# Optimization experiments

Hardware: AMD Instinct MI355X
Metric: run time of the kernel (lower is better)

The kernel has to match this reference:

```python
import jax, jax.numpy as jnp
import numpy as np

N_LINKS = 100000
N_EDGES = 1600000
D = 64          # link_state_dim
RU = 256        # readout_units
G = 256         # number of graphs
T = 4           # message passing iterations


def _glorot(key, shape):
    fan_in, fan_out = shape[0], shape[1]
    limit = np.sqrt(6.0 / (fan_in + fan_out)).astype(np.float32)
    return jax.random.uniform(key, shape, jnp.float32, -limit, limit)


def setup_inputs() -> dict:
    key = jax.random.key(0)
    ks = jax.random.split(key, 12)
    states_action = jax.random.normal(ks[0], (N_LINKS, D), jnp.float32)
    states_graph_ids = jnp.sort(jax.random.randint(ks[1], (N_LINKS,), 0, G))
    states_first = jax.random.randint(ks[2], (N_EDGES,), 0, N_LINKS)
    states_second = jax.random.randint(ks[3], (N_EDGES,), 0, N_LINKS)
    # Message: Dense(2D -> D) with selu
    W_msg = _glorot(ks[4], (2 * D, D)); b_msg = jnp.zeros((D,), jnp.float32)
    # GCN: Linear(D -> D) + relu, then unsorted_segment_sum
    W_gcn = _glorot(ks[5], (D, D)); b_gcn = jnp.zeros((D,), jnp.float32)
    # Readout MLP: D -> RU -> RU -> 1
    W_r1 = _glorot(ks[6], (D, RU)); b_r1 = jnp.zeros((RU,), jnp.float32)
    W_r2 = _glorot(ks[7], (RU, RU)); b_r2 = jnp.zeros((RU,), jnp.float32)
    W_r3 = _glorot(ks[8], (RU, 1)); b_r3 = jnp.zeros((1,), jnp.float32)
    return {
        "states_action": states_action,
        "W_msg": W_msg, "b_msg": b_msg,
        "W_gcn": W_gcn, "b_gcn": b_gcn,
        "W_r1": W_r1, "b_r1": b_r1,
        "W_r2": W_r2, "b_r2": b_r2,
        "W_r3": W_r3, "b_r3": b_r3,
        "states_graph_ids": states_graph_ids,
        "states_first": states_first,
        "states_second": states_second,
        "sates_num_edges": N_EDGES,
    }


def reference(states_action, W_msg, b_msg, W_gcn, b_gcn,
              W_r1, b_r1, W_r2, b_r2, W_r3, b_r3,
              states_graph_ids, states_first, states_second, sates_num_edges):
    n_links = states_action.shape[0]
    link_state = states_action
    for _ in range(T):
        main_e = link_state[states_first]      # [E, D]
        neigh_e = link_state[states_second]    # [E, D]
        concat = jnp.concatenate([main_e, neigh_e], axis=1)  # [E, 2D]
        msg = jax.nn.selu(concat @ W_msg + b_msg)            # [E, D]
        h = jax.nn.relu(msg @ W_gcn + b_gcn)                 # [E, D]
        # scatter-add messages back onto links (segment ids = states_second)
        link_state = jax.ops.segment_sum(h, states_second, num_segments=n_links)
        # dropout rate is 0.0 -> identity
    # per-graph readout (graph ids are sorted, fixed G segments)
    graph_emb = jax.ops.segment_sum(link_state, states_graph_ids, num_segments=G)
    r = jax.nn.selu(graph_emb @ W_r1 + b_r1)
    r = jax.nn.selu(r @ W_r2 + b_r2)
    r = r @ W_r3 + b_r3                                      # [G, 1]
    return r
```

## Files before the change

### kernel.cpp

```cpp
#include <hip/hip_runtime.h>
#include <hip/hip_bf16.h>
#include <math.h>

#define D 64
#define RU 256
#define CHUNK 8
#define QSTRIDE 68
#define BIN_SHIFT 7
#define NSB 256

#if __has_builtin(__builtin_amdgcn_exp2f)
#define EXP2F(x) __builtin_amdgcn_exp2f(x)
#else
#define EXP2F(x) exp2f(x)
#endif

typedef short bf16x8 __attribute__((ext_vector_type(8)));
typedef float f32x4 __attribute__((ext_vector_type(4)));

__device__ __forceinline__ float selu_f(float x) {
    return x > 0.0f ? 1.0507009873554805f * x
                    : 1.7580993408473766f * (__expf(x) - 1.0f);
}

__device__ __forceinline__ float selu_x2(float x2) {
    const float p = fmaxf(x2, 0.0f);
    const float n = fminf(x2, 0.0f);
    const float e = EXP2F(n);
    return fmaf(1.7580993408473766f, e, fmaf(0.72829042516f, p, -1.7580993408473766f));
}

__device__ __forceinline__ short f2bf_rtne(float x) {
    union { float f; unsigned u; } v; v.f = x;
    unsigned r = (v.u + 0x7FFFu + ((v.u >> 16) & 1u)) >> 16;
    return (short)r;
}
__device__ __forceinline__ float bf2f(short s) {
    union { float f; unsigned u; } v; v.u = ((unsigned)(unsigned short)s) << 16;
    return v.f;
}
__device__ __forceinline__ unsigned packpair(float a, float b) {
    float2 p; p.x = a; p.y = b;
    __hip_bfloat162 hb = __float22bfloat162_rn(p);
    return *(unsigned*)&hb;
}

__device__ __forceinline__ bf16x8 pack8(const float* v) {
    union { bf16x8 v; unsigned u[4]; } H;
#pragma unroll
    for (int j = 0; j < 4; ++j) H.u[j] = packpair(v[2 * j], v[2 * j + 1]);
    return H.v;
}

#define FIDX(ks, jt, qd, m) ((((((ks) * 4 + (jt)) * 4 + (qd)) * 16) + (m)) * 8)

__global__ __launch_bounds__(256) void wprep_kernel(
    const float* __restrict__ W_msg, const float* __restrict__ W_gcn,
    const float* __restrict__ b_gcn,
    unsigned short* __restrict__ WAh, unsigned short* __restrict__ WAl,
    unsigned short* __restrict__ WBh, unsigned short* __restrict__ WBl,
    unsigned short* __restrict__ WGh, float* __restrict__ cstar,
    unsigned short* __restrict__ Pb, int n_links)
{
    const float LOG2E = 1.4426950408889634f;
    const int t = blockIdx.x * 256 + threadIdx.x;

    if (blockIdx.x == 0 && threadIdx.x < 64) {
        const int col = threadIdx.x;
        Pb[(size_t)n_links * 64 + col] = 0xFF80;
        const float c0 = bf2f(f2bf_rtne(-1.7580993408473766f));
        float acc = b_gcn[col];
        for (int k = 0; k < 64; ++k)
            acc = fmaf(c0, bf2f(f2bf_rtne(W_gcn[k * 64 + col])), acc);
        cstar[col] = fmaxf(acc, 0.0f);
    }

    if (t >= 4096) return;
    const int i  = t & 7;
    const int m  = (t >> 3) & 15;
    const int qd = (t >> 7) & 3;
    const int jt = (t >> 9) & 3;
    const int ks = t >> 11;
    const int kk = ks * 32 + qd * 8 + i;
    const int nn = jt * 16 + m;

    float w = W_msg[kk * 64 + nn] * LOG2E;
    short hi = f2bf_rtne(w);
    WAh[t] = (unsigned short)hi;
    WAl[t] = (unsigned short)f2bf_rtne(w - bf2f(hi));

    w = W_msg[(64 + kk) * 64 + nn] * LOG2E;
    hi = f2bf_rtne(w);
    WBh[t] = (unsigned short)hi;
    WBl[t] = (unsigned short)f2bf_rtne(w - bf2f(hi));

    WGh[t] = (unsigned short)f2bf_rtne(W_gcn[kk * 64 + nn]);
}

__global__ __launch_bounds__(256) void s2bf_kernel(
    const float* __restrict__ in, unsigned short* __restrict__ out, int n4)
{
    for (int i = blockIdx.x * 256 + threadIdx.x; i < n4; i += gridDim.x * 256) {
        const float4 v = ((const float4*)in)[i];
        uint2 o;
        o.x = packpair(v.x, v.y);
        o.y = packpair(v.z, v.w);
        ((uint2*)out)[i] = o;
    }
}


__global__ __launch_bounds__(256) void histA_kernel(
    const int* __restrict__ second, int* __restrict__ ghist,
    int n_edges, int nbins)
{
    __shared__ int lhist[1024];
    for (int i = threadIdx.x; i < nbins; i += 256) lhist[i] = 0;
    __syncthreads();
    const int per = (n_edges + gridDim.x - 1) / gridDim.x;
    const int e0 = blockIdx.x * per;
    const int e1 = min(e0 + per, n_edges);
    for (int e = e0 + threadIdx.x; e < e1; e += 256)
        atomicAdd(&lhist[second[e] >> BIN_SHIFT], 1);
    __syncthreads();
    for (int i = threadIdx.x; i < nbins; i += 256)
        ghist[i * gridDim.x + blockIdx.x] = lhist[i];
}

__global__ __launch_bounds__(64) void sumbins_kernel(
    int* __restrict__ ghist, int* __restrict__ btot, int nbins)
{
    const int b = blockIdx.x, tid = threadIdx.x;
    int d[4], p[4];
#pragma unroll
    for (int k = 0; k < 4; ++k) {
        d[k] = ghist[b * NSB + k * 64 + tid];
        p[k] = d[k];
    }
#pragma unroll
    for (int off = 1; off < 64; off <<= 1) {
#pragma unroll
        for (int k = 0; k < 4; ++k) {
            const int t = __shfl_up(p[k], off, 64);
            if (tid >= off) p[k] += t;
        }
    }
    int base = 0;
#pragma unroll
    for (int k = 0; k < 4; ++k) {
        const int tot = __shfl(p[k], 63, 64);
        ghist[b * NSB + k * 64 + tid] = base + p[k] - d[k];
        base += tot;
    }
    if (tid == 63) btot[b] = base;
}

__global__ __launch_bounds__(1024) void scanS_kernel(int* __restrict__ data, int n)
{
    __shared__ int wsum[16], woff[16];
    const int tid = threadIdx.x, wave = tid >> 6, lane = tid & 63;
    const int x = (tid < n) ? data[tid] : 0;
    int v = x;
#pragma unroll
    for (int off = 1; off < 64; off <<= 1) {
        const int t = __shfl_up(v, off, 64);
        if (lane >= off) v += t;
    }
    if (lane == 63) wsum[wave] = v;
    __syncthreads();
    if (wave == 0) {
        int s = (lane < 16) ? wsum[lane] : 0;
#pragma unroll
        for (int off = 1; off < 16; off <<= 1) {
            const int t = __shfl_up(s, off, 64);
            if (lane >= off) s += t;
        }
        if (lane < 16) woff[lane] = s - wsum[lane];
    }
    __syncthreads();
    if (tid < n) data[tid] = woff[wave] + v - x;
}

__global__ __launch_bounds__(256) void scatterC_kernel(
    const int* __restrict__ first, const int* __restrict__ second,
    const int* __restrict__ ghist, const int* __restrict__ btot,
    unsigned* __restrict__ tmp, int n_edges, int nbins)
{
    __shared__ int lcur[1024];
    for (int i = threadIdx.x; i < nbins; i += 256)
        lcur[i] = ghist[i * NSB + blockIdx.x] + btot[i];
    __syncthreads();
    const int per = (n_edges + gridDim.x - 1) / gridDim.x;
    const int e0 = blockIdx.x * per;
    const int e1 = min(e0 + per, n_edges);
    for (int e = e0 + threadIdx.x; e < e1; e += 256) {
        const int s = second[e];
        const int pos = atomicAdd(&lcur[s >> BIN_SHIFT], 1);
        tmp[pos] = (unsigned)first[e] | ((unsigned)(s & 127) << 20);
    }
}

__global__ __launch_bounds__(256) void binsortD_kernel(
    const unsigned* __restrict__ tmp, const int* __restrict__ btot,
    int* __restrict__ sfirst, int* __restrict__ row_ptr, int* __restrict__ ptot,
    int n_edges, int n_links, int nbins)
{
    __shared__ int ldeg[128];
    __shared__ int lpre[128];
    __shared__ int lcur[128];
    const int b = blockIdx.x;
    const int tid = threadIdx.x;
    const int lbase = b << BIN_SHIFT;
    const int nl = min(128, n_links - lbase);
    const int eb = btot[b];
    const int ee = (b + 1 < nbins) ? btot[b + 1] : n_edges;

    if (tid < 128) ldeg[tid] = 0;
    __syncthreads();
    for (int e = eb + tid; e < ee; e += 256)
        atomicAdd(&ldeg[tmp[e] >> 20], 1);
    __syncthreads();
    if (tid < 64) {
        const int d0 = ldeg[tid], d1 = ldeg[64 + tid];
        int p0 = d0, p1 = d1;
#pragma unroll
        for (int off = 1; off < 64; off <<= 1) {
            const int t0 = __shfl_up(p0, off, 64);
            const int t1 = __shfl_up(p1, off, 64);
            if (tid >= off) { p0 += t0; p1 += t1; }
        }
        const int tot0 = __shfl(p0, 63, 64);
        lpre[tid] = p0 - d0;
        lpre[64 + tid] = tot0 + p1 - d1;
        const int n0 = (d0 + 15) >> 4, n1 = (d1 + 15) >> 4;
        int q0 = n0, q1 = n1;
#pragma unroll
        for (int off = 1; off < 64; off <<= 1) {
            const int t0 = __shfl_up(q0, off, 64);
            const int t1 = __shfl_up(q1, off, 64);
            if (tid >= off) { q0 += t0; q1 += t1; }
        }
        if (tid == 63) ptot[b] = q0 + q1;
    }
    __syncthreads();
    if (tid < nl) row_ptr[lbase + tid] = eb + lpre[tid];
    if (b == nbins - 1 && tid == 0) row_ptr[n_links] = n_edges;
    if (tid < 128) lcur[tid] = lpre[tid];
    __syncthreads();
    for (int e = eb + tid; e < ee; e += 256) {
        const unsigned v = tmp[e];
        const int pos = eb + atomicAdd(&lcur[v >> 20], 1);
        sfirst[pos] = (int)(v & 0xFFFFFu);
    }
    if (b == 0)
        for (int i = tid; i < 64; i += 256) sfirst[n_edges + i] = 0;
}

__global__ __launch_bounds__(256) void tbuild_kernel(
    const int* __restrict__ row_ptr, const int* __restrict__ tbase,
    int* __restrict__ ptile, int* __restrict__ tinfo,
    int n_links, int nbins)
{
    __shared__ int rpl[130];
    __shared__ int ltp[130];
    const int b = blockIdx.x, tid = threadIdx.x;
    const int lbase = b << BIN_SHIFT;
    const int nl = min(128, n_links - lbase);
    if (tid <= nl) rpl[tid] = row_ptr[lbase + tid];
    __syncthreads();
    if (tid < 64) {
        const int d0 = (tid < nl) ? rpl[tid + 1] - rpl[tid] : 0;
        const int d1 = (64 + tid < nl) ? rpl[64 + tid + 1] - rpl[64 + tid] : 0;
        const int n0 = (d0 + 15) >> 4, n1 = (d1 + 15) >> 4;
        int p0 = n0, p1 = n1;
#pragma unroll
        for (int off = 1; off < 64; off <<= 1) {
            const int t0 = __shfl_up(p0, off, 64);
            const int t1 = __shfl_up(p1, off, 64);
            if (tid >= off) { p0 += t0; p1 += t1; }
        }
        const int tot0 = __shfl(p0, 63, 64);
        ltp[tid] = p0 - n0;
        ltp[64 + tid] = tot0 + p1 - n1;
        if (tid == 63) ltp[128] = tot0 + p1;
    }
    __syncthreads();
    const int tb = tbase[b];
    if (tid <= nl) ptile[lbase + tid] = tb + ltp[tid];
    const int ntb = ltp[128];
    for (int tl = tid; tl < ntb; tl += 256) {
        int lo = 0, hi = nl - 1;
        while (lo < hi) {
            const int mid = (lo + hi + 1) >> 1;
            if (ltp[mid] <= tl) lo = mid; else hi = mid - 1;
        }
        const int li = lo;
        const int eo = rpl[li] + ((tl - ltp[li]) << 4);
        const int rend = rpl[li + 1];
        const int vc = min(16, rend - eo);
        const int last = (eo + 16 >= rend) ? 1 : 0;
        tinfo[tb + tl] = eo | ((li & 7) << 21) | (last << 24) | (vc << 25);
    }
    if (b == nbins - 1 && tid < 8) tinfo[tb + ntb + tid] = 0;
}

__global__ __launch_bounds__(256) void growfind_kernel(
    const int* __restrict__ gid, int* __restrict__ grow, int n_links, int G)
{
    const int g = blockIdx.x * blockDim.x + threadIdx.x;
    if (g > G) return;
    if (g == G) { grow[G] = n_links; return; }
    int lo = 0, hi = n_links;
    while (lo < hi) {
        const int mid = (lo + hi) >> 1;
        if (gid[mid] < g) lo = mid + 1; else hi = mid;
    }
    grow[g] = lo;
}

__global__ __launch_bounds__(256) void p_mfma_kernel(
    const unsigned short* __restrict__ Sb,
    const unsigned short* __restrict__ WAh, const unsigned short* __restrict__ WAl,
    unsigned short* __restrict__ P, int n_links)
{
    const int tid = threadIdx.x;
    const int wave = tid >> 6;
    const int lane = tid & 63;
    const int m = lane & 15;
    const int qd = lane >> 4;

    bf16x8 Bh[2][4], Bl[2][4];
#pragma unroll
    for (int ks = 0; ks < 2; ++ks)
#pragma unroll
        for (int jt = 0; jt < 4; ++jt) {
            const int off = FIDX(ks, jt, qd, m);
            Bh[ks][jt] = *(const bf16x8*)(WAh + off);
            Bl[ks][jt] = *(const bf16x8*)(WAl + off);
        }
    const bf16x8 z = (bf16x8){0, 0, 0, 0, 0, 0, 0, 0};

    const int ngroups = (n_links + 63) >> 6;
    for (int g = blockIdx.x; g < ngroups; g += gridDim.x) {
        const int base = g * 64 + wave * 16;
        const int l = base + m;
        bf16x8 Ah0 = z, Ah1 = z;
        if (l < n_links) {
            Ah0 = *(const bf16x8*)(Sb + (size_t)l * D + qd * 8);
            Ah1 = *(const bf16x8*)(Sb + (size_t)l * D + 32 + qd * 8);
        }
        f32x4 accP[4];
#pragma unroll
        for (int jt = 0; jt < 4; ++jt) {
            accP[jt] = (f32x4){0.f, 0.f, 0.f, 0.f};
            accP[jt] = __builtin_amdgcn_mfma_f32_16x16x32_bf16(Ah0, Bh[0][jt], accP[jt], 0, 0, 0);
            accP[jt] = __builtin_amdgcn_mfma_f32_16x16x32_bf16(Ah0, Bl[0][jt], accP[jt], 0, 0, 0);
            accP[jt] = __builtin_amdgcn_mfma_f32_16x16x32_bf16(Ah1, Bh[1][jt], accP[jt], 0, 0, 0);
            accP[jt] = __builtin_amdgcn_mfma_f32_16x16x32_bf16(Ah1, Bl[1][jt], accP[jt], 0, 0, 0);
        }
#pragma unroll
        for (int r = 0; r < 4; ++r) {
            const int lr = base + qd * 4 + r;
            if (lr < n_links) {
#pragma unroll
                for (int jt = 0; jt < 4; ++jt)
                    P[(size_t)lr * D + jt * 16 + m] =
                        (unsigned short)f2bf_rtne(accP[jt][r]);
            }
        }
    }
}

__global__ __launch_bounds__(256, 4) void edge_link_kernel(
    unsigned short* __restrict__ Sb, const unsigned short* __restrict__ P,
    const int* __restrict__ sfirst, const int* __restrict__ tinfo,
    const int* __restrict__ ptile,
    const float* __restrict__ b_msg,
    const unsigned short* __restrict__ WBh, const unsigned short* __restrict__ WBl,
    const unsigned short* __restrict__ WGh,
    const float* __restrict__ b_gcn, const float* __restrict__ cstar,
    int n_links)
{
    __shared__ float qt[4][CHUNK * QSTRIDE + 4];
    __shared__ float cbl[64];
    const int tid = threadIdx.x;
    const int wave = tid >> 6;
    const int lane = tid & 63;
    const int m = lane & 15;
    const int qd = lane >> 4;

    cbl[lane] = cstar[lane];

    const int l0 = (blockIdx.x * 4 + wave) * CHUNK;
    if (l0 >= n_links) return;
    const int nl = min(CHUNK, n_links - l0);

    const float LOG2E = 1.4426950408889634f;
    float bmsgC[4];
#pragma unroll
    for (int jt = 0; jt < 4; ++jt) bmsgC[jt] = b_msg[jt * 16 + m] * LOG2E;

    {
        const bf16x8 z = (bf16x8){0, 0, 0, 0, 0, 0, 0, 0};
        const int l = l0 + m;
        bf16x8 Ah0 = z, Ah1 = z;
        if ((l < n_links) && (m < CHUNK)) {
            Ah0 = *(const bf16x8*)(Sb + (size_t)l * D + qd * 8);
            Ah1 = *(const bf16x8*)(Sb + (size_t)l * D + 32 + qd * 8);
        }
        f32x4 accQ[4];
#pragma unroll
        for (int jt = 0; jt < 4; ++jt) accQ[jt] = (f32x4){0.f, 0.f, 0.f, 0.f};
#pragma unroll
        for (int ks = 0; ks < 2; ++ks) {
            bf16x8 WbH[4], WbL[4];
#pragma unroll
            for (int jt = 0; jt < 4; ++jt) {
                const int off = FIDX(ks, jt, qd, m);
                WbH[jt] = *(const bf16x8*)(WBh + off);
                WbL[jt] = *(const bf16x8*)(WBl + off);
            }
            const bf16x8 A = ks ? Ah1 : Ah0;
#pragma unroll
            for (int jt = 0; jt < 4; ++jt) {
                accQ[jt] = __builtin_amdgcn_mfma_f32_16x16x32_bf16(A, WbH[jt], accQ[jt], 0, 0, 0);
                accQ[jt] = __builtin_amdgcn_mfma_f32_16x16x32_bf16(A, WbL[jt], accQ[jt], 0, 0, 0);
            }
        }
#pragma unroll
        for (int r = 0; r < 4; ++r) {
            const int row = qd * 4 + r;
            if (row < CHUNK) {
#pragma unroll
                for (int jt = 0; jt < 4; ++jt)
                    qt[wave][row * QSTRIDE + jt * 16 + m] = accQ[jt][r] + bmsgC[jt];
            }
        }
    }

    bf16x8 Gh[2][4];
#pragma unroll
    for (int ks = 0; ks < 2; ++ks)
#pragma unroll
        for (int jt = 0; jt < 4; ++jt)
            Gh[ks][jt] = *(const bf16x8*)(WGh + FIDX(ks, jt, qd, m));

    float bias_gcn[4];
#pragma unroll
    for (int jt = 0; jt < 4; ++jt) bias_gcn[jt] = b_gcn[jt * 16 + m];

    const int tpv = ptile[l0 + min(lane, nl)];
#pragma unroll
    for (int i = 0; i < CHUNK; ++i) {
        if (i < nl && __shfl(tpv, i + 1, 64) == __shfl(tpv, i, 64))
            Sb[(size_t)(l0 + i) * D + lane] = 0;
    }
    const int tbeg = __builtin_amdgcn_readfirstlane(tpv);
    const int tend = __builtin_amdgcn_readfirstlane(__shfl(tpv, nl, 64));
    if (tbeg >= tend) return;

    int ti0 = tinfo[tbeg];
    int ti1 = tinfo[tbeg + 1];
    int ti2 = tinfo[tbeg + 2];

    bf16x8 p00, p01;
    {
        const int eo = ti0 & 0x1FFFFF, vc = (ti0 >> 25) & 31;
        int sf = sfirst[eo + m];
        sf = (m < vc) ? sf : n_links;
        const unsigned short* Pr = P + (size_t)sf * D;
        p00 = *(const bf16x8*)(Pr + qd * 8);
        p01 = *(const bf16x8*)(Pr + 32 + qd * 8);
    }
    int sf1;
    {
        const int eo = ti1 & 0x1FFFFF, vc = (ti1 >> 25) & 31;
        int sf = sfirst[eo + m];
        sf1 = (m < vc) ? sf : n_links;
    }

    float qb[16];
    int qli = -1;
    float rsum[4] = {0.f, 0.f, 0.f, 0.f};

    for (int t = tbeg; t < tend; ++t) {
        const int tiN = tinfo[t + 3];
        const int eo2 = ti2 & 0x1FFFFF, vc2 = (ti2 >> 25) & 31;
        int sf2 = sfirst[eo2 + m];
        sf2 = (m < vc2) ? sf2 : n_links;
        const unsigned short* Pr1 = P + (size_t)sf1 * D;
        const bf16x8 p10 = *(const bf16x8*)(Pr1 + qd * 8);
        const bf16x8 p11 = *(const bf16x8*)(Pr1 + 32 + qd * 8);

        const int li0 = (ti0 >> 21) & 7;
        const int vc0 = (ti0 >> 25) & 31;

        if (li0 != qli) {
            qli = li0;
            const int qoff = li0 * QSTRIDE + qd * 8;
            *(float4*)&qb[0]  = *(const float4*)&qt[wave][qoff];
            *(float4*)&qb[4]  = *(const float4*)&qt[wave][qoff + 4];
            *(float4*)&qb[8]  = *(const float4*)&qt[wave][qoff + 32];
            *(float4*)&qb[12] = *(const float4*)&qt[wave][qoff + 36];
        }

        float msgA[8];
#pragma unroll
        for (int i = 0; i < 8; ++i)
            msgA[i] = selu_x2(bf2f(p00[i]) + qb[i]);
        const bf16x8 Ah0 = pack8(msgA);
        float msgB[8];
#pragma unroll
        for (int i = 0; i < 8; ++i)
            msgB[i] = selu_x2(bf2f(p01[i]) + qb[8 + i]);
        const bf16x8 Ah1 = pack8(msgB);

        f32x4 acc[4];
#pragma unroll
        for (int jt = 0; jt < 4; ++jt) {
            const float b = bias_gcn[jt];
            acc[jt] = (f32x4){b, b, b, b};
            acc[jt] = __builtin_amdgcn_mfma_f32_16x16x32_bf16(Ah0, Gh[0][jt], acc[jt], 0, 0, 0);
            acc[jt] = __builtin_amdgcn_mfma_f32_16x16x32_bf16(Ah1, Gh[1][jt], acc[jt], 0, 0, 0);
        }
#pragma unroll
        for (int jt = 0; jt < 4; ++jt)
#pragma unroll
            for (int r = 0; r < 4; ++r)
                rsum[jt] += fmaxf(acc[jt][r], 0.0f);

        if (ti0 & (1 << 24)) {
            const int over = qd * 4 + 4 - vc0;
            const float cnt = (float)max(0, min(4, over));
#pragma unroll
            for (int jt = 0; jt < 4; ++jt) {
                rsum[jt] -= cbl[jt * 16 + m] * cnt;
                rsum[jt] += __shfl_xor(rsum[jt], 16, 64);
                rsum[jt] += __shfl_xor(rsum[jt], 32, 64);
            }
            const float outv = (qd == 0) ? rsum[0] : (qd == 1) ? rsum[1]
                             : (qd == 2) ? rsum[2] : rsum[3];
            Sb[(size_t)(l0 + li0) * D + lane] = (unsigned short)f2bf_rtne(outv);
#pragma unroll
            for (int jt = 0; jt < 4; ++jt) rsum[jt] = 0.0f;
        }

        ti0 = ti1; ti1 = ti2; ti2 = tiN;
        sf1 = sf2;
        p00 = p10; p01 = p11;
    }
}

__global__ __launch_bounds__(256) void gsum8_kernel(
    const unsigned short* __restrict__ Sb, const int* __restrict__ grow,
    float* __restrict__ gemb)
{
    __shared__ float red[4][64];
    const int g = blockIdx.x >> 3;
    const int slice = blockIdx.x & 7;
    const int slot = threadIdx.x >> 6;
    const int j = threadIdx.x & 63;
    const int ls = grow[g], le = grow[g + 1];
    float acc = 0.0f;
    for (int l = ls + slice * 4 + slot; l < le; l += 32)
        acc += bf2f((short)Sb[(size_t)l * D + j]);
    red[slot][j] = acc;
    __syncthreads();
    if (slot == 0)
        atomicAdd(&gemb[g * D + j], red[0][j] + red[1][j] + red[2][j] + red[3][j]);
}

__global__ __launch_bounds__(256) void mlp_kernel(
    const float* __restrict__ gemb,
    const float* __restrict__ W_r1, const float* __restrict__ b_r1,
    const float* __restrict__ W_r2, const float* __restrict__ b_r2,
    const float* __restrict__ W_r3, const float* __restrict__ b_r3,
    float* __restrict__ out)
{
    __shared__ float gl[64];
    __shared__ float row1[RU];
    __shared__ float row2[RU];
    __shared__ float fin[4];
    const int g = blockIdx.x;
    const int tid = threadIdx.x;
    const int slot = tid >> 6;
    const int lane = tid & 63;

    if (tid < 64) gl[tid] = gemb[g * D + tid];
    __syncthreads();

    float a1 = b_r1[tid];
#pragma unroll 8
    for (int k = 0; k < 64; ++k) a1 += gl[k] * W_r1[k * RU + tid];
    row1[tid] = selu_f(a1);
    __syncthreads();

    float a2 = b_r2[tid];
#pragma unroll 8
    for (int k = 0; k < RU; ++k) a2 += row1[k] * W_r2[k * RU + tid];
    row2[tid] = selu_f(a2);
    __syncthreads();

    float p = row2[tid] * W_r3[tid];
#pragma unroll
    for (int off = 32; off >= 1; off >>= 1)
        p += __shfl_down(p, off, 64);
    if (lane == 0) fin[slot] = p;
    __syncthreads();
    if (tid == 0)
        out[g] = fin[0] + fin[1] + fin[2] + fin[3] + b_r3[0];
}

extern "C" void kernel_launch(void* const* d_in, const int* in_sizes, int n_in,
                              void* d_out, int out_size, void* d_ws, size_t ws_size,
                              hipStream_t stream)
{
    const float* states_action = (const float*)d_in[0];
    const float* W_msg = (const float*)d_in[1];
    const float* b_msg = (const float*)d_in[2];
    const float* W_gcn = (const float*)d_in[3];
    const float* b_gcn = (const float*)d_in[4];
    const float* W_r1 = (const float*)d_in[5];
    const float* b_r1 = (const float*)d_in[6];
    const float* W_r2 = (const float*)d_in[7];
    const float* b_r2 = (const float*)d_in[8];
    const float* W_r3 = (const float*)d_in[9];
    const float* b_r3 = (const float*)d_in[10];
    const int* gid = (const int*)d_in[11];
    const int* first = (const int*)d_in[12];
    const int* second = (const int*)d_in[13];

    const int n_links = in_sizes[0] / D;
    const int n_edges = in_sizes[12];
    const int G = out_size;
    const int nbins = (n_links + 127) >> BIN_SHIFT;

    char* ws2 = (char*)d_ws;
    auto alloc = [&](size_t bytes) {
        char* p = ws2; ws2 += (bytes + 63) & ~(size_t)63; return p;
    };
    unsigned short* Sb = (unsigned short*)alloc((size_t)n_links * D * 2);
    unsigned short* Pb = (unsigned short*)alloc((size_t)(n_links + 1) * D * 2);
    float* gemb = (float*)alloc((size_t)G * D * sizeof(float));
    int* row_ptr = (int*)alloc((size_t)(n_links + 1) * sizeof(int));
    int* grow = (int*)alloc((size_t)(G + 1) * sizeof(int));
    unsigned* tmp = (unsigned*)alloc((size_t)n_edges * sizeof(unsigned));
    int* sfirst = (int*)alloc((size_t)(n_edges + 64) * sizeof(int));
    unsigned short* WAh = (unsigned short*)alloc(4096 * 2);
    unsigned short* WAl = (unsigned short*)alloc(4096 * 2);
    unsigned short* WBh = (unsigned short*)alloc(4096 * 2);
    unsigned short* WBl = (unsigned short*)alloc(4096 * 2);
    unsigned short* WGh = (unsigned short*)alloc(4096 * 2);
    int* btot = (int*)alloc((size_t)nbins * sizeof(int));
    int* ptotv = (int*)alloc((size_t)nbins * sizeof(int));
    int* ptile = (int*)alloc((size_t)(n_links + 1) * sizeof(int));
    float* cstar = (float*)alloc(64 * sizeof(float));
    int* tinfoA = (int*)tmp;
    int* ghist = (int*)sfirst;

    hipMemsetAsync(gemb, 0, (size_t)G * D * sizeof(float), stream);
    s2bf_kernel<<<1024, 256, 0, stream>>>(states_action, Sb, n_links * D / 4);
    wprep_kernel<<<16, 256, 0, stream>>>(W_msg, W_gcn, b_gcn, WAh, WAl, WBh, WBl,
                                         WGh, cstar, Pb, n_links);
    histA_kernel<<<NSB, 256, 0, stream>>>(second, ghist, n_edges, nbins);
    sumbins_kernel<<<nbins, 64, 0, stream>>>(ghist, btot, nbins);
    scanS_kernel<<<1, 1024, 0, stream>>>(btot, nbins);
    scatterC_kernel<<<NSB, 256, 0, stream>>>(first, second, ghist, btot, tmp,
                                             n_edges, nbins);
    binsortD_kernel<<<nbins, 256, 0, stream>>>(tmp, btot, sfirst, row_ptr, ptotv,
                                               n_edges, n_links, nbins);
    scanS_kernel<<<1, 1024, 0, stream>>>(ptotv, nbins);
    tbuild_kernel<<<nbins, 256, 0, stream>>>(row_ptr, ptotv, ptile, tinfoA,
                                             n_links, nbins);
    growfind_kernel<<<2, 256, 0, stream>>>(gid, grow, n_links, G);

    const int edge_blocks = (n_links + 4 * CHUNK - 1) / (4 * CHUNK);
    for (int t = 0; t < 4; ++t) {
        p_mfma_kernel<<<1024, 256, 0, stream>>>(Sb, WAh, WAl, Pb, n_links);
        edge_link_kernel<<<edge_blocks, 256, 0, stream>>>(Sb, Pb, sfirst, tinfoA,
                                                          ptile, b_msg, WBh, WBl,
                                                          WGh, b_gcn, cstar,
                                                          n_links);
    }

    gsum8_kernel<<<G * 8, 256, 0, stream>>>(Sb, grow, gemb);
    mlp_kernel<<<G, 256, 0, stream>>>(gemb, W_r1, b_r1, W_r2, b_r2,
                                      W_r3, b_r3, (float*)d_out);
}
```

Baseline: 521.8 us.

## Replace per-link tile table with contiguous 16-edge tiles over each chunk's CSR range

Drops the tile-info build, which needed an extra scan and the tbuild kernel, and the padding-correction constant. Each wave now walks its 8-link chunk's edge range in dense 16-edge tiles that may span link boundaries. Each edge's local link index, carried in sfirst bits 20-22, masks the per-row ReLU accumulation. This removes two preprocessing launches and wastes fewer MFMA rows on padding, but adds per-tile shuffles, per-row compares and a boundary-flush loop inside the hot loop.

```diff
diff --git a/kernel.cpp b/kernel.cpp
--- a/kernel.cpp
+++ b/kernel.cpp
@@ -56,25 +56,12 @@
 
 __global__ __launch_bounds__(256) void wprep_kernel(
     const float* __restrict__ W_msg, const float* __restrict__ W_gcn,
-    const float* __restrict__ b_gcn,
     unsigned short* __restrict__ WAh, unsigned short* __restrict__ WAl,
     unsigned short* __restrict__ WBh, unsigned short* __restrict__ WBl,
-    unsigned short* __restrict__ WGh, float* __restrict__ cstar,
-    unsigned short* __restrict__ Pb, int n_links)
+    unsigned short* __restrict__ WGh)
 {
     const float LOG2E = 1.4426950408889634f;
     const int t = blockIdx.x * 256 + threadIdx.x;
-
-    if (blockIdx.x == 0 && threadIdx.x < 64) {
-        const int col = threadIdx.x;
-        Pb[(size_t)n_links * 64 + col] = 0xFF80;
-        const float c0 = bf2f(f2bf_rtne(-1.7580993408473766f));
-        float acc = b_gcn[col];
-        for (int k = 0; k < 64; ++k)
-            acc = fmaf(c0, bf2f(f2bf_rtne(W_gcn[k * 64 + col])), acc);
-        cstar[col] = fmaxf(acc, 0.0f);
-    }
-
     if (t >= 4096) return;
     const int i  = t & 7;
     const int m  = (t >> 3) & 15;
@@ -202,7 +189,7 @@
 
 __global__ __launch_bounds__(256) void binsortD_kernel(
     const unsigned* __restrict__ tmp, const int* __restrict__ btot,
-    int* __restrict__ sfirst, int* __restrict__ row_ptr, int* __restrict__ ptot,
+    int* __restrict__ sfirst, int* __restrict__ row_ptr,
     int n_edges, int n_links, int nbins)
 {
     __shared__ int ldeg[128];
@@ -232,15 +219,6 @@
         const int tot0 = __shfl(p0, 63, 64);
         lpre[tid] = p0 - d0;
         lpre[64 + tid] = tot0 + p1 - d1;
-        const int n0 = (d0 + 15) >> 4, n1 = (d1 + 15) >> 4;
-        int q0 = n0, q1 = n1;
-#pragma unroll
-        for (int off = 1; off < 64; off <<= 1) {
-            const int t0 = __shfl_up(q0, off, 64);
-            const int t1 = __shfl_up(q1, off, 64);
-            if (tid >= off) { q0 += t0; q1 += t1; }
-        }
-        if (tid == 63) ptot[b] = q0 + q1;
     }
     __syncthreads();
     if (tid < nl) row_ptr[lbase + tid] = eb + lpre[tid];
@@ -250,58 +228,10 @@
     for (int e = eb + tid; e < ee; e += 256) {
         const unsigned v = tmp[e];
         const int pos = eb + atomicAdd(&lcur[v >> 20], 1);
-        sfirst[pos] = (int)(v & 0xFFFFFu);
+        sfirst[pos] = (int)(v & 0x7FFFFFu);
     }
     if (b == 0)
         for (int i = tid; i < 64; i += 256) sfirst[n_edges + i] = 0;
-}
-
-__global__ __launch_bounds__(256) void tbuild_kernel(
-    const int* __restrict__ row_ptr, const int* __restrict__ tbase,
-    int* __restrict__ ptile, int* __restrict__ tinfo,
-    int n_links, int nbins)
-{
-    __shared__ int rpl[130];
-    __shared__ int ltp[130];
-    const int b = blockIdx.x, tid = threadIdx.x;
-    const int lbase = b << BIN_SHIFT;
-    const int nl = min(128, n_links - lbase);
-    if (tid <= nl) rpl[tid] = row_ptr[lbase + tid];
-    __syncthreads();
-    if (tid < 64) {
-        const int d0 = (tid < nl) ? rpl[tid + 1] - rpl[tid] : 0;
-        const int d1 = (64 + tid < nl) ? rpl[64 + tid + 1] - rpl[64 + tid] : 0;
-        const int n0 = (d0 + 15) >> 4, n1 = (d1 + 15) >> 4;
-        int p0 = n0, p1 = n1;
-#pragma unroll
-        for (int off = 1; off < 64; off <<= 1) {
-            const int t0 = __shfl_up(p0, off, 64);
-            const int t1 = __shfl_up(p1, off, 64);
-            if (tid >= off) { p0 += t0; p1 += t1; }
-        }
-        const int tot0 = __shfl(p0, 63, 64);
-        ltp[tid] = p0 - n0;
-        ltp[64 + tid] = tot0 + p1 - n1;
-        if (tid == 63) ltp[128] = tot0 + p1;
-    }
-    __syncthreads();
-    const int tb = tbase[b];
-    if (tid <= nl) ptile[lbase + tid] = tb + ltp[tid];
-    const int ntb = ltp[128];
-    for (int tl = tid; tl < ntb; tl += 256) {
-        int lo = 0, hi = nl - 1;
-        while (lo < hi) {
-            const int mid = (lo + hi + 1) >> 1;
-            if (ltp[mid] <= tl) lo = mid; else hi = mid - 1;
-        }
-        const int li = lo;
-        const int eo = rpl[li] + ((tl - ltp[li]) << 4);
-        const int rend = rpl[li + 1];
-        const int vc = min(16, rend - eo);
-        const int last = (eo + 16 >= rend) ? 1 : 0;
-        tinfo[tb + tl] = eo | ((li & 7) << 21) | (last << 24) | (vc << 25);
-    }
-    if (b == nbins - 1 && tid < 8) tinfo[tb + ntb + tid] = 0;
 }
 
 __global__ __launch_bounds__(256) void growfind_kernel(
@@ -373,23 +303,19 @@
 
 __global__ __launch_bounds__(256, 4) void edge_link_kernel(
     unsigned short* __restrict__ Sb, const unsigned short* __restrict__ P,
-    const int* __restrict__ sfirst, const int* __restrict__ tinfo,
-    const int* __restrict__ ptile,
+    const int* __restrict__ sfirst, const int* __restrict__ row_ptr,
     const float* __restrict__ b_msg,
     const unsigned short* __restrict__ WBh, const unsigned short* __restrict__ WBl,
     const unsigned short* __restrict__ WGh,
-    const float* __restrict__ b_gcn, const float* __restrict__ cstar,
+    const float* __restrict__ b_gcn,
     int n_links)
 {
     __shared__ float qt[4][CHUNK * QSTRIDE + 4];
-    __shared__ float cbl[64];
     const int tid = threadIdx.x;
     const int wave = tid >> 6;
     const int lane = tid & 63;
     const int m = lane & 15;
     const int qd = lane >> 4;
-
-    cbl[lane] = cstar[lane];
 
     const int l0 = (blockIdx.x * 4 + wave) * CHUNK;
     if (l0 >= n_links) return;
@@ -449,60 +375,45 @@
 #pragma unroll
     for (int jt = 0; jt < 4; ++jt) bias_gcn[jt] = b_gcn[jt * 16 + m];
 
-    const int tpv = ptile[l0 + min(lane, nl)];
-#pragma unroll
-    for (int i = 0; i < CHUNK; ++i) {
-        if (i < nl && __shfl(tpv, i + 1, 64) == __shfl(tpv, i, 64))
+    const int rpv = row_ptr[l0 + min(lane, nl)];
+#define RP(i) __shfl(rpv, (i), 64)
+    const int eb = __builtin_amdgcn_readfirstlane(RP(0));
+    const int ee = __builtin_amdgcn_readfirstlane(RP(nl));
+    if (eb >= ee) {
+        for (int i = 0; i < nl; ++i)
             Sb[(size_t)(l0 + i) * D + lane] = 0;
-    }
-    const int tbeg = __builtin_amdgcn_readfirstlane(tpv);
-    const int tend = __builtin_amdgcn_readfirstlane(__shfl(tpv, nl, 64));
-    if (tbeg >= tend) return;
-
-    int ti0 = tinfo[tbeg];
-    int ti1 = tinfo[tbeg + 1];
-    int ti2 = tinfo[tbeg + 2];
-
+        return;
+    }
+    const int ntiles = (ee - eb + 15) >> 4;
+
+    int sv0 = sfirst[eb + m];
+    int sv1 = sfirst[eb + 16 + m];
     bf16x8 p00, p01;
     {
-        const int eo = ti0 & 0x1FFFFF, vc = (ti0 >> 25) & 31;
-        int sf = sfirst[eo + m];
-        sf = (m < vc) ? sf : n_links;
-        const unsigned short* Pr = P + (size_t)sf * D;
+        const unsigned short* Pr = P + (size_t)(sv0 & 0xFFFFF) * D;
         p00 = *(const bf16x8*)(Pr + qd * 8);
         p01 = *(const bf16x8*)(Pr + 32 + qd * 8);
     }
-    int sf1;
-    {
-        const int eo = ti1 & 0x1FFFFF, vc = (ti1 >> 25) & 31;
-        int sf = sfirst[eo + m];
-        sf1 = (m < vc) ? sf : n_links;
-    }
-
-    float qb[16];
-    int qli = -1;
+
+    int bcur = 0;
     float rsum[4] = {0.f, 0.f, 0.f, 0.f};
-
-    for (int t = tbeg; t < tend; ++t) {
-        const int tiN = tinfo[t + 3];
-        const int eo2 = ti2 & 0x1FFFFF, vc2 = (ti2 >> 25) & 31;
-        int sf2 = sfirst[eo2 + m];
-        sf2 = (m < vc2) ? sf2 : n_links;
-        const unsigned short* Pr1 = P + (size_t)sf1 * D;
+    int eo = eb;
+
+    for (int t = 0; t < ntiles; ++t, eo += 16) {
+        const int sv2 = sfirst[eo + 32 + m];
+        const unsigned short* Pr1 = P + (size_t)(sv1 & 0xFFFFF) * D;
         const bf16x8 p10 = *(const bf16x8*)(Pr1 + qd * 8);
         const bf16x8 p11 = *(const bf16x8*)(Pr1 + 32 + qd * 8);
 
-        const int li0 = (ti0 >> 21) & 7;
-        const int vc0 = (ti0 >> 25) & 31;
-
-        if (li0 != qli) {
-            qli = li0;
-            const int qoff = li0 * QSTRIDE + qd * 8;
-            *(float4*)&qb[0]  = *(const float4*)&qt[wave][qoff];
-            *(float4*)&qb[4]  = *(const float4*)&qt[wave][qoff + 4];
-            *(float4*)&qb[8]  = *(const float4*)&qt[wave][qoff + 32];
-            *(float4*)&qb[12] = *(const float4*)&qt[wave][qoff + 36];
-        }
+        const bool valid = (eo + m < ee);
+        const int limv = valid ? ((sv0 >> 20) & 7) : 8;
+        const int qoff = (valid ? ((sv0 >> 20) & 7) : 0) * QSTRIDE + qd * 8;
+
+        float qb[16];
+        *(float4*)&qb[0]  = *(const float4*)&qt[wave][qoff];
+        *(float4*)&qb[4]  = *(const float4*)&qt[wave][qoff + 4];
+        *(float4*)&qb[8]  = *(const float4*)&qt[wave][qoff + 32];
+        *(float4*)&qb[12] = *(const float4*)&qt[wave][qoff + 36];
 
         float msgA[8];
 #pragma unroll
@@ -523,32 +434,48 @@
             acc[jt] = __builtin_amdgcn_mfma_f32_16x16x32_bf16(Ah0, Gh[0][jt], acc[jt], 0, 0, 0);
             acc[jt] = __builtin_amdgcn_mfma_f32_16x16x32_bf16(Ah1, Gh[1][jt], acc[jt], 0, 0, 0);
         }
-#pragma unroll
-        for (int jt = 0; jt < 4; ++jt)
-#pragma unroll
-            for (int r = 0; r < 4; ++r)
-                rsum[jt] += fmaxf(acc[jt][r], 0.0f);
-
-        if (ti0 & (1 << 24)) {
-            const int over = qd * 4 + 4 - vc0;
-            const float cnt = (float)max(0, min(4, over));
+
+        const int lr0 = __shfl(limv, qd * 4 + 0, 64);
+        const int lr1 = __shfl(limv, qd * 4 + 1, 64);
+        const int lr2 = __shfl(limv, qd * 4 + 2, 64);
+        const int lr3 = __shfl(limv, qd * 4 + 3, 64);
+
+        while (true) {
+            const int b0 = bcur;
 #pragma unroll
             for (int jt = 0; jt < 4; ++jt) {
-                rsum[jt] -= cbl[jt * 16 + m] * cnt;
-                rsum[jt] += __shfl_xor(rsum[jt], 16, 64);
-                rsum[jt] += __shfl_xor(rsum[jt], 32, 64);
+                rsum[jt] += fmaxf((lr0 == b0) ? acc[jt][0] : 0.0f, 0.0f);
+                rsum[jt] += fmaxf((lr1 == b0) ? acc[jt][1] : 0.0f, 0.0f);
+                rsum[jt] += fmaxf((lr2 == b0) ? acc[jt][2] : 0.0f, 0.0f);
+                rsum[jt] += fmaxf((lr3 == b0) ? acc[jt][3] : 0.0f, 0.0f);
             }
-            const float outv = (qd == 0) ? rsum[0] : (qd == 1) ? rsum[1]
-                             : (qd == 2) ? rsum[2] : rsum[3];
-            Sb[(size_t)(l0 + li0) * D + lane] = (unsigned short)f2bf_rtne(outv);
-#pragma unroll
-            for (int jt = 0; jt < 4; ++jt) rsum[jt] = 0.0f;
-        }
-
-        ti0 = ti1; ti1 = ti2; ti2 = tiN;
-        sf1 = sf2;
+            if (bcur < nl && RP(bcur + 1) <= eo + 16) {
+#pragma unroll
+                for (int jt = 0; jt < 4; ++jt) {
+                    rsum[jt] += __shfl_xor(rsum[jt], 16, 64);
+                    rsum[jt] += __shfl_xor(rsum[jt], 32, 64);
+                }
+                const float outv = (qd == 0) ? rsum[0] : (qd == 1) ? rsum[1]
+                                 : (qd == 2) ? rsum[2] : rsum[3];
+                Sb[(size_t)(l0 + bcur) * D + lane] = (unsigned short)f2bf_rtne(outv);
+#pragma unroll
+                for (int jt = 0; jt < 4; ++jt) rsum[jt] = 0.0f;
+                ++bcur;
+                if (bcur >= nl) break;
+            } else {
+                break;
+            }
+        }
+
+        sv0 = sv1; sv1 = sv2;
         p00 = p10; p01 = p11;
     }
+
+    while (bcur < nl) {
+        Sb[(size_t)(l0 + bcur) * D + lane] = 0;
+        ++bcur;
+    }
+#undef RP
 }
 
 __global__ __launch_bounds__(256) void gsum8_kernel(
@@ -640,7 +567,7 @@
         char* p = ws2; ws2 += (bytes + 63) & ~(size_t)63; return p;
     };
     unsigned short* Sb = (unsigned short*)alloc((size_t)n_links * D * 2);
-    unsigned short* Pb = (unsigned short*)alloc((size_t)(n_links + 1) * D * 2);
+    unsigned short* Pb = (unsigned short*)alloc((size_t)n_links * D * 2);
     float* gemb = (float*)alloc((size_t)G * D * sizeof(float));
     int* row_ptr = (int*)alloc((size_t)(n_links + 1) * sizeof(int));
     int* grow = (int*)alloc((size_t)(G + 1) * sizeof(int));
@@ -652,35 +579,26 @@
     unsigned short* WBl = (unsigned short*)alloc(4096 * 2);
     unsigned short* WGh = (unsigned short*)alloc(4096 * 2);
     int* btot = (int*)alloc((size_t)nbins * sizeof(int));
-    int* ptotv = (int*)alloc((size_t)nbins * sizeof(int));
-    int* ptile = (int*)alloc((size_t)(n_links + 1) * sizeof(int));
-    float* cstar = (float*)alloc(64 * sizeof(float));
-    int* tinfoA = (int*)tmp;
     int* ghist = (int*)sfirst;
 
     hipMemsetAsync(gemb, 0, (size_t)G * D * sizeof(float), stream);
     s2bf_kernel<<<1024, 256, 0, stream>>>(states_action, Sb, n_links * D / 4);
-    wprep_kernel<<<16, 256, 0, stream>>>(W_msg, W_gcn, b_gcn, WAh, WAl, WBh, WBl,
-                                         WGh, cstar, Pb, n_links);
+    wprep_kernel<<<16, 256, 0, stream>>>(W_msg, W_gcn, WAh, WAl, WBh, WBl, WGh);
     histA_kernel<<<NSB, 256, 0, stream>>>(second, ghist, n_edges, nbins);
     sumbins_kernel<<<nbins, 64, 0, stream>>>(ghist, btot, nbins);
     scanS_kernel<<<1, 1024, 0, stream>>>(btot, nbins);
     scatterC_kernel<<<NSB, 256, 0, stream>>>(first, second, ghist, btot, tmp,
                                              n_edges, nbins);
-    binsortD_kernel<<<nbins, 256, 0, stream>>>(tmp, btot, sfirst, row_ptr, ptotv,
+    binsortD_kernel<<<nbins, 256, 0, stream>>>(tmp, btot, sfirst, row_ptr,
                                                n_edges, n_links, nbins);
-    scanS_kernel<<<1, 1024, 0, stream>>>(ptotv, nbins);
-    tbuild_kernel<<<nbins, 256, 0, stream>>>(row_ptr, ptotv, ptile, tinfoA,
-                                             n_links, nbins);
     growfind_kernel<<<2, 256, 0, stream>>>(gid, grow, n_links, G);
 
     const int edge_blocks = (n_links + 4 * CHUNK - 1) / (4 * CHUNK);
     for (int t = 0; t < 4; ++t) {
         p_mfma_kernel<<<1024, 256, 0, stream>>>(Sb, WAh, WAl, Pb, n_links);
-        edge_link_kernel<<<edge_blocks, 256, 0, stream>>>(Sb, Pb, sfirst, tinfoA,
-                                                          ptile, b_msg, WBh, WBl,
-                                                          WGh, b_gcn, cstar,
-                                                          n_links);
+        edge_link_kernel<<<edge_blocks, 256, 0, stream>>>(Sb, Pb, sfirst, row_ptr,
+                                                          b_msg, WBh, WBl, WGh,
+                                                          b_gcn, n_links);
     }
 
     gsum8_kernel<<<G * 8, 256, 0, stream>>>(Sb, grow, gemb);
```

After: 477.4 us. -8.5%, faster.
